# Optimization experiments

Hardware: AMD Instinct MI355X
Metric: run time of the kernel (lower is better)

Reference implementation:

```python
import jax, jax.numpy as jnp
import numpy as np

B, L, D = 1, 4096, 1024
N_AR, N_DIFF, D_HEAD = 8, 8, 64
H = N_AR + N_DIFF
ROPE_BASE = 10000.0


def rotate_half(x):
    x1, x2 = jnp.split(x, 2, axis=-1)
    return jnp.concatenate([-x2, x1], axis=-1)


def rope_cos_sin(seq_len, d_head):
    inv_freq = 1.0 / (ROPE_BASE ** (jnp.arange(0, d_head, 2, dtype=jnp.float32) / d_head))
    t = jnp.arange(seq_len, dtype=jnp.float32)
    freqs = t[:, None] * inv_freq[None, :]          # [L, d_head//2]
    emb = jnp.concatenate([freqs, freqs], axis=-1)  # [L, d_head]
    return jnp.cos(emb), jnp.sin(emb)


def setup_inputs() -> dict:
    key = jax.random.key(0)
    ks = jax.random.split(key, 5)
    return {
        "hidden_states": jax.random.normal(ks[0], (B, L, D), dtype=jnp.float32),
        "Wq": jax.random.normal(ks[1], (D, H * D_HEAD), dtype=jnp.float32) * 0.02,
        "Wk": jax.random.normal(ks[2], (D, H * D_HEAD), dtype=jnp.float32) * 0.02,
        "Wv": jax.random.normal(ks[3], (D, H * D_HEAD), dtype=jnp.float32) * 0.02,
        "Wo": jax.random.normal(ks[4], (H * D_HEAD, D), dtype=jnp.float32) * 0.02,
    }


def _attend(q, k, v, mask):
    # q,k,v: [B, h, L, d]; mask: [L, L] additive
    scale = D_HEAD ** -0.5
    scores = jnp.einsum("bhqd,bhkd->bhqk", q, k) * scale + mask
    attn = jax.nn.softmax(scores.astype(jnp.float32), axis=-1).astype(q.dtype)
    return jnp.einsum("bhqk,bhkd->bhqd", attn, v)


def reference(hidden_states, Wq, Wk, Wv, Wo):
    b, l, _ = hidden_states.shape

    def heads(x, W):
        return (x @ W).reshape(b, l, H, D_HEAD).transpose(0, 2, 1, 3)  # [B,H,L,d]

    q = heads(hidden_states, Wq)
    k = heads(hidden_states, Wk)
    v = heads(hidden_states, Wv)

    cos, sin = rope_cos_sin(l, D_HEAD)  # [L, d]
    q = q * cos + rotate_half(q) * sin
    k = k * cos + rotate_half(k) * sin

    neg_inf = jnp.finfo(jnp.float32).min
    causal = jnp.where(jnp.tril(jnp.ones((l, l), dtype=bool)), 0.0, -jnp.inf).astype(jnp.float32)

    out_ar = _attend(q[:, :N_AR], k[:, :N_AR], v[:, :N_AR], causal)
    out_diff = _attend(q[:, N_AR:], k[:, N_AR:], v[:, N_AR:], jnp.zeros((l, l), jnp.float32))

    out = jnp.concatenate([out_ar, out_diff], axis=1)          # [B,H,L,d]
    out = out.transpose(0, 2, 1, 3).reshape(b, l, H * D_HEAD)  # [B,L,H*d]
    return out @ Wo
```

## Files before the change

kernel.cpp:

```cpp
#include <hip/hip_runtime.h>

#define LSEQ 4096
#define DMODEL 1024
#define HTOT 16
#define NAR 8
#define DHEAD 64
#define QKVS 3072

typedef unsigned short u16;
typedef unsigned int u32;
typedef __attribute__((ext_vector_type(8))) short bf16x8;
typedef __attribute__((ext_vector_type(4))) short bf16x4;
typedef __attribute__((ext_vector_type(4))) float f32x4;
typedef __attribute__((ext_vector_type(4))) unsigned int u32x4;

typedef __attribute__((address_space(1))) void gvoid;
typedef __attribute__((address_space(3))) void lvoid;

__device__ __forceinline__ void cp16(const void* g, void* l) {
    __builtin_amdgcn_global_load_lds((gvoid*)(void*)g, (lvoid*)l, 16, 0, 0);
}

__device__ __forceinline__ float bfs(u16 v) { return __uint_as_float((u32)v << 16); }
__device__ __forceinline__ u16 f2bf(float f) {
    u32 x = __float_as_uint(f);
    return (u16)((x + 0x7fffu + ((x >> 16) & 1u)) >> 16);
}
__device__ __forceinline__ u32 packtr(float lo, float hi) {
    return __builtin_amdgcn_perm(__float_as_uint(hi), __float_as_uint(lo), 0x07060302u);
}

__global__ __launch_bounds__(256) void transp_cvt3(
    const float* __restrict__ Wq, const float* __restrict__ Wk,
    const float* __restrict__ Wv, u16* __restrict__ D)
{
    __shared__ u16 T[64][72];
    const float* S = (blockIdx.z == 0) ? Wq : ((blockIdx.z == 1) ? Wk : Wv);
    u16* Dz = D + (size_t)blockIdx.z * 1024 * 1024;
    const int tid = threadIdx.x;
    const int bx = blockIdx.x, by = blockIdx.y;
#pragma unroll
    for (int i = 0; i < 4; ++i) {
        int id = tid + i * 256;
        int fr = id >> 4, fc = id & 15;
        float4 v = *(const float4*)(S + (size_t)(by * 64 + fr) * 1024 + bx * 64 + fc * 4);
        T[fc * 4 + 0][fr] = f2bf(v.x);
        T[fc * 4 + 1][fr] = f2bf(v.y);
        T[fc * 4 + 2][fr] = f2bf(v.z);
        T[fc * 4 + 3][fr] = f2bf(v.w);
    }
    __syncthreads();
#pragma unroll
    for (int i = 0; i < 2; ++i) {
        int id = tid + i * 256;
        int c = id >> 3, g = id & 7;
        *(uint4*)(Dz + (size_t)(bx * 64 + c) * 1024 + by * 64 + g * 8) = *(const uint4*)&T[c][g * 8];
    }
}

__global__ __launch_bounds__(256) void transp_cvt(
    const float* __restrict__ S, u16* __restrict__ D)
{
    __shared__ u16 T[64][72];
    const int tid = threadIdx.x;
    const int bx = blockIdx.x, by = blockIdx.y;
#pragma unroll
    for (int i = 0; i < 4; ++i) {
        int id = tid + i * 256;
        int fr = id >> 4, fc = id & 15;
        float4 v = *(const float4*)(S + (size_t)(by * 64 + fr) * 1024 + bx * 64 + fc * 4);
        T[fc * 4 + 0][fr] = f2bf(v.x);
        T[fc * 4 + 1][fr] = f2bf(v.y);
        T[fc * 4 + 2][fr] = f2bf(v.z);
        T[fc * 4 + 3][fr] = f2bf(v.w);
    }
    __syncthreads();
#pragma unroll
    for (int i = 0; i < 2; ++i) {
        int id = tid + i * 256;
        int c = id >> 3, g = id & 7;
        *(uint4*)(D + (size_t)(bx * 64 + c) * 1024 + by * 64 + g * 8) = *(const uint4*)&T[c][g * 8];
    }
}

__global__ __launch_bounds__(256) void gemm_qkv(
    const float* __restrict__ A, const u16* __restrict__ Bt, u16* __restrict__ C)
{
    __shared__ u16 As[2][128][40];
    __shared__ u16 Bs[2][128][32];
    const int tid = threadIdx.x;
    const int lane = tid & 63, w = tid >> 6;
    const int col = lane & 15, quad = lane >> 4;
    const int bm = blockIdx.y << 7, bn = blockIdx.x << 7;
    const int wm = (w & 1) << 6, wn = (w >> 1) << 6;
    const int sr = lane >> 2, sc = (lane & 3) << 3;
    const int ar0 = tid >> 2, ag = (tid & 3) << 3;
    const f32x4 zero = {0.f, 0.f, 0.f, 0.f};
    f32x4 acc[4][4];
#pragma unroll
    for (int i = 0; i < 4; ++i)
#pragma unroll
        for (int j = 0; j < 4; ++j) acc[i][j] = zero;

    {
#pragma unroll
        for (int i = 0; i < 2; ++i)
            cp16(Bt + (size_t)(bn + w * 32 + i * 16 + sr) * 1024 + sc, &Bs[0][w * 32 + i * 16][0]);
#pragma unroll
        for (int it = 0; it < 2; ++it) {
            const float* ap = A + (size_t)(bm + ar0 + it * 64) * 1024 + ag;
            float4 a0 = *(const float4*)ap;
            float4 a1 = *(const float4*)(ap + 4);
            uint4 pk;
            pk.x = packtr(a0.x, a0.y); pk.y = packtr(a0.z, a0.w);
            pk.z = packtr(a1.x, a1.y); pk.w = packtr(a1.z, a1.w);
            *(uint4*)&As[0][ar0 + it * 64][ag] = pk;
        }
    }

    for (int kc = 0; kc < 32; ++kc) {
        const int cur = kc & 1, nxt = cur ^ 1;
        __syncthreads();
        const bool pre = (kc + 1 < 32);
        float4 a0[2], a1[2];
        if (pre) {
            const int k1 = (kc + 1) * 32;
#pragma unroll
            for (int i = 0; i < 2; ++i)
                cp16(Bt + (size_t)(bn + w * 32 + i * 16 + sr) * 1024 + k1 + sc,
                     &Bs[nxt][w * 32 + i * 16][0]);
#pragma unroll
            for (int it = 0; it < 2; ++it) {
                const float* ap = A + (size_t)(bm + ar0 + it * 64) * 1024 + k1 + ag;
                a0[it] = *(const float4*)ap;
                a1[it] = *(const float4*)(ap + 4);
            }
        }
        bf16x8 af[4], bfr[4];
#pragma unroll
        for (int i = 0; i < 4; ++i) af[i] = *(const bf16x8*)&As[cur][wm + i * 16 + col][quad * 8];
#pragma unroll
        for (int j = 0; j < 4; ++j) bfr[j] = *(const bf16x8*)&Bs[cur][wn + j * 16 + col][quad * 8];
#pragma unroll
        for (int i = 0; i < 4; ++i)
#pragma unroll
            for (int j = 0; j < 4; ++j)
                acc[i][j] = __builtin_amdgcn_mfma_f32_16x16x32_bf16(af[i], bfr[j], acc[i][j], 0, 0, 0);
        if (pre) {
#pragma unroll
            for (int it = 0; it < 2; ++it) {
                uint4 pk;
                pk.x = packtr(a0[it].x, a0[it].y); pk.y = packtr(a0[it].z, a0[it].w);
                pk.z = packtr(a1[it].x, a1[it].y); pk.w = packtr(a1[it].z, a1[it].w);
                *(uint4*)&As[nxt][ar0 + it * 64][ag] = pk;
            }
        }
    }

    if (blockIdx.x < 16) {
        const float scale = (blockIdx.x < 8) ? 0.18033688011112042f : 1.0f;
        const float inv0 = __expf((float)col * -0.2878231366242557f);
        const float inv1 = __expf((float)(16 + col) * -0.2878231366242557f);
#pragma unroll
        for (int i = 0; i < 4; ++i)
#pragma unroll
            for (int r = 0; r < 4; ++r) {
                const float t = (float)(bm + wm + i * 16 + quad * 4 + r);
                float s0, c0, s1, c1;
                __sincosf(t * inv0, &s0, &c0);
                __sincosf(t * inv1, &s1, &c1);
                float a0 = acc[i][0][r], b0 = acc[i][2][r];
                acc[i][0][r] = (a0 * c0 - b0 * s0) * scale;
                acc[i][2][r] = (b0 * c0 + a0 * s0) * scale;
                float a1 = acc[i][1][r], b1 = acc[i][3][r];
                acc[i][1][r] = (a1 * c1 - b1 * s1) * scale;
                acc[i][3][r] = (b1 * c1 + a1 * s1) * scale;
            }
    }
#pragma unroll
    for (int i = 0; i < 4; ++i)
#pragma unroll
        for (int j = 0; j < 4; ++j)
#pragma unroll
            for (int r = 0; r < 4; ++r)
                C[(size_t)(bm + wm + i * 16 + quad * 4 + r) * QKVS + bn + wn + j * 16 + col] =
                    f2bf(acc[i][j][r]);
}

__global__ __launch_bounds__(256) void gemm_out(
    const u16* __restrict__ A, const u16* __restrict__ Bt, float* __restrict__ C)
{
    __shared__ u16 As[2][128][32];
    __shared__ u16 Bs[2][128][32];
    const int tid = threadIdx.x;
    const int lane = tid & 63, w = tid >> 6;
    const int col = lane & 15, quad = lane >> 4;
    const int bm = blockIdx.y << 7, bn = blockIdx.x << 7;
    const int wm = (w & 1) << 6, wn = (w >> 1) << 6;
    const int sr = lane >> 2, sc = (lane & 3) << 3;
    const f32x4 zero = {0.f, 0.f, 0.f, 0.f};
    f32x4 acc[4][4];
#pragma unroll
    for (int i = 0; i < 4; ++i)
#pragma unroll
        for (int j = 0; j < 4; ++j) acc[i][j] = zero;

#pragma unroll
    for (int i = 0; i < 2; ++i) {
        const int r0 = w * 32 + i * 16;
        cp16(A  + (size_t)(bm + r0 + sr) * 1024 + sc, &As[0][r0][0]);
        cp16(Bt + (size_t)(bn + r0 + sr) * 1024 + sc, &Bs[0][r0][0]);
    }

    for (int kc = 0; kc < 32; ++kc) {
        const int cur = kc & 1, nxt = cur ^ 1;
        __syncthreads();
        if (kc + 1 < 32) {
            const int k1 = (kc + 1) * 32;
#pragma unroll
            for (int i = 0; i < 2; ++i) {
                const int r0 = w * 32 + i * 16;
                cp16(A  + (size_t)(bm + r0 + sr) * 1024 + k1 + sc, &As[nxt][r0][0]);
                cp16(Bt + (size_t)(bn + r0 + sr) * 1024 + k1 + sc, &Bs[nxt][r0][0]);
            }
        }
        bf16x8 af[4], bfr[4];
#pragma unroll
        for (int i = 0; i < 4; ++i) af[i] = *(const bf16x8*)&As[cur][wm + i * 16 + col][quad * 8];
#pragma unroll
        for (int j = 0; j < 4; ++j) bfr[j] = *(const bf16x8*)&Bs[cur][wn + j * 16 + col][quad * 8];
#pragma unroll
        for (int i = 0; i < 4; ++i)
#pragma unroll
            for (int j = 0; j < 4; ++j)
                acc[i][j] = __builtin_amdgcn_mfma_f32_16x16x32_bf16(af[i], bfr[j], acc[i][j], 0, 0, 0);
    }
#pragma unroll
    for (int i = 0; i < 4; ++i)
#pragma unroll
        for (int j = 0; j < 4; ++j)
#pragma unroll
            for (int r = 0; r < 4; ++r)
                C[(size_t)(bm + wm + i * 16 + quad * 4 + r) * 1024 + bn + wn + j * 16 + col] =
                    acc[i][j][r];
}

__global__ __launch_bounds__(256) void attn_mfma(
    const u16* __restrict__ QKV, u16* __restrict__ AO)
{
    __shared__ u16 Ks[2][128][64];
    __shared__ u16 Vt[2][64][136];
    const int bid = blockIdx.x;
    int h, qt;
    if (bid < 256) { h = 8 + (bid & 7); qt = bid >> 3; }
    else { int i = bid - 256; h = i & 7; qt = 31 - (i >> 3); }
    const bool causal = (h < NAR);
    const int tid = threadIdx.x;
    const int w = tid >> 6, lane = tid & 63;
    const int col = lane & 15, quad = lane >> 4;
    const int qb = qt * 128;
    const int qr0 = qb + w * 32 + col;
    const int qr1 = qr0 + 16;
    const int cva = ((lane >> 1) & 3) * 32 + (lane >> 3) * 4 + (lane & 1) * 2;

    bf16x8 qf[2][2];
#pragma unroll
    for (int s = 0; s < 2; ++s)
#pragma unroll
        for (int ks = 0; ks < 2; ++ks)
            qf[s][ks] = *(const bf16x8*)(QKV + (size_t)(qr0 + s * 16) * QKVS +
                                         h * DHEAD + ks * 32 + quad * 8);

    bf16x8 ones8;
#pragma unroll
    for (int i = 0; i < 8; ++i) ones8[i] = (short)0x3F80;

    const f32x4 zero = {0.f, 0.f, 0.f, 0.f};
    f32x4 O[2][5];
#pragma unroll
    for (int s = 0; s < 2; ++s)
#pragma unroll
        for (int nd = 0; nd < 5; ++nd) O[s][nd] = zero;

    const int nch = causal ? (qt + 1) : (LSEQ / 128);
    const int krow = lane >> 3;
    const int kcb = (lane & 7) ^ krow;
    const u16* kbase = QKV + (size_t)krow * QKVS + 1024 + h * DHEAD + kcb * 8;
    const u16* vbase = QKV + (size_t)(lane * 2) * QKVS + 2048 + h * DHEAD + w * 16;

    u32x4 vA0, vA1, vB0, vB1;
    bf16x8 pf8[2][4];

#define VT_WRITE(CUR)                                                                              \
    _Pragma("unroll")                                                                              \
    for (int j = 0; j < 4; ++j) {                                                                  \
        *(u32*)&Vt[CUR][w * 16 + 2 * j][cva]         = __builtin_amdgcn_perm(vB0[j], vA0[j], 0x05040100u); \
        *(u32*)&Vt[CUR][w * 16 + 2 * j + 1][cva]     = __builtin_amdgcn_perm(vB0[j], vA0[j], 0x07060302u); \
        *(u32*)&Vt[CUR][w * 16 + 8 + 2 * j][cva]     = __builtin_amdgcn_perm(vB1[j], vA1[j], 0x05040100u); \
        *(u32*)&Vt[CUR][w * 16 + 8 + 2 * j + 1][cva] = __builtin_amdgcn_perm(vB1[j], vA1[j], 0x07060302u); \
    }

#define PV_STEP(PRV)                                                                               \
    {                                                                                              \
        __builtin_amdgcn_s_setprio(1);                                                             \
        _Pragma("unroll")                                                                          \
        for (int tp = 0; tp < 4; ++tp) {                                                           \
            bf16x8 vv[4];                                                                          \
            _Pragma("unroll")                                                                      \
            for (int nd = 0; nd < 4; ++nd)                                                         \
                vv[nd] = *(const bf16x8*)&Vt[PRV][nd * 16 + col][quad * 32 + tp * 8];              \
            _Pragma("unroll")                                                                      \
            for (int nd = 0; nd < 4; ++nd) {                                                       \
                O[0][nd] = __builtin_amdgcn_mfma_f32_16x16x32_bf16(vv[nd], pf8[0][tp], O[0][nd], 0, 0, 0); \
                O[1][nd] = __builtin_amdgcn_mfma_f32_16x16x32_bf16(vv[nd], pf8[1][tp], O[1][nd], 0, 0, 0); \
            }                                                                                      \
            O[0][4] = __builtin_amdgcn_mfma_f32_16x16x32_bf16(ones8, pf8[0][tp], O[0][4], 0, 0, 0); \
            O[1][4] = __builtin_amdgcn_mfma_f32_16x16x32_bf16(ones8, pf8[1][tp], O[1][4], 0, 0, 0); \
        }                                                                                          \
        __builtin_amdgcn_s_setprio(0);                                                             \
    }

#define S_STEP(KBUF, CH)                                                                           \
    {                                                                                              \
        const bool mask = causal && ((CH) == qt);                                                  \
        _Pragma("unroll")                                                                          \
        for (int hf = 0; hf < 2; ++hf) {                                                           \
            f32x4 st[2][4];                                                                        \
            _Pragma("unroll")                                                                      \
            for (int s = 0; s < 2; ++s)                                                            \
                _Pragma("unroll")                                                                  \
                for (int jj = 0; jj < 4; ++jj) st[s][jj] = zero;                                   \
            __builtin_amdgcn_s_setprio(1);                                                         \
            _Pragma("unroll")                                                                      \
            for (int ks = 0; ks < 2; ++ks)                                                         \
                _Pragma("unroll")                                                                  \
                for (int jj = 0; jj < 4; ++jj) {                                                   \
                    bf16x8 kf = *(const bf16x8*)&Ks[KBUF][(hf * 4 + jj) * 16 + col]                \
                                                         [((ks * 4 + quad) ^ (col & 7)) * 8];      \
                    st[0][jj] = __builtin_amdgcn_mfma_f32_16x16x32_bf16(kf, qf[0][ks], st[0][jj], 0, 0, 0); \
                    st[1][jj] = __builtin_amdgcn_mfma_f32_16x16x32_bf16(kf, qf[1][ks], st[1][jj], 0, 0, 0); \
                }                                                                                  \
            __builtin_amdgcn_s_setprio(0);                                                         \
            if (mask) {                                                                            \
                _Pragma("unroll")                                                                  \
                for (int jj = 0; jj < 4; ++jj) {                                                   \
                    const int kk = (CH) * 128 + (hf * 4 + jj) * 16 + quad * 4;                     \
                    _Pragma("unroll")                                                              \
                    for (int r = 0; r < 4; ++r) {                                                  \
                        if (kk + r > qr0) st[0][jj][r] = -1e30f;                                   \
                        if (kk + r > qr1) st[1][jj][r] = -1e30f;                                   \
                    }                                                                              \
                }                                                                                  \
            }                                                                                      \
            _Pragma("unroll")                                                                      \
            for (int s = 0; s < 2; ++s)                                                            \
                _Pragma("unroll")                                                                  \
                for (int jj = 0; jj < 4; ++jj) {                                                   \
                    u32 plo = packtr(__builtin_amdgcn_exp2f(st[s][jj][0]),                         \
                                     __builtin_amdgcn_exp2f(st[s][jj][1]));                        \
                    u32 phi = packtr(__builtin_amdgcn_exp2f(st[s][jj][2]),                         \
                                     __builtin_amdgcn_exp2f(st[s][jj][3]));                        \
                    u32* p = (u32*)&pf8[s][0] + (hf * 4 + jj) * 2;                                 \
                    p[0] = plo; p[1] = phi;                                                        \
                }                                                                                  \
        }                                                                                          \
    }

#pragma unroll
    for (int i = 0; i < 4; ++i)
        cp16(kbase + (size_t)((i * 4 + w) * 8) * QKVS, &Ks[0][(i * 4 + w) * 8][0]);
    vA0 = *(u32x4*)(vbase);
    vA1 = *(u32x4*)(vbase + 8);
    vB0 = *(u32x4*)(vbase + QKVS);
    vB1 = *(u32x4*)(vbase + QKVS + 8);
    __syncthreads();
    VT_WRITE(0);
    if (nch > 1) {
#pragma unroll
        for (int i = 0; i < 4; ++i)
            cp16(kbase + (size_t)(128 + (i * 4 + w) * 8) * QKVS, &Ks[1][(i * 4 + w) * 8][0]);
        const u16* vp = vbase + (size_t)128 * QKVS;
        vA0 = *(u32x4*)(vp);
        vA1 = *(u32x4*)(vp + 8);
        vB0 = *(u32x4*)(vp + QKVS);
        vB1 = *(u32x4*)(vp + QKVS + 8);
    }
    S_STEP(0, 0);

    for (int ch = 1; ch < nch; ++ch) {
        const int cur = ch & 1, prv = cur ^ 1;
        __syncthreads();
        VT_WRITE(cur);
        if (ch + 1 < nch) {
            const size_t c1 = (size_t)(ch + 1) * 128;
#pragma unroll
            for (int i = 0; i < 4; ++i)
                cp16(kbase + (c1 + (i * 4 + w) * 8) * QKVS, &Ks[prv][(i * 4 + w) * 8][0]);
            const u16* vp = vbase + c1 * QKVS;
            vA0 = *(u32x4*)(vp);
            vA1 = *(u32x4*)(vp + 8);
            vB0 = *(u32x4*)(vp + QKVS);
            vB1 = *(u32x4*)(vp + QKVS + 8);
        }
        PV_STEP(prv);
        S_STEP(cur, ch);
    }

    __syncthreads();
    {
        const int prv = (nch - 1) & 1;
        PV_STEP(prv);
    }
#pragma unroll
    for (int s = 0; s < 2; ++s) {
        const float inv = 1.f / O[s][4][0];
        const int qrow = qr0 + s * 16;
#pragma unroll
        for (int nd = 0; nd < 4; ++nd) {
            ushort4 ov;
            ov.x = f2bf(O[s][nd][0] * inv);
            ov.y = f2bf(O[s][nd][1] * inv);
            ov.z = f2bf(O[s][nd][2] * inv);
            ov.w = f2bf(O[s][nd][3] * inv);
            *(ushort4*)(AO + (size_t)qrow * 1024 + h * DHEAD + nd * 16 + quad * 4) = ov;
        }
    }
#undef VT_WRITE
#undef PV_STEP
#undef S_STEP
}

extern "C" void kernel_launch(void* const* d_in, const int* in_sizes, int n_in,
                              void* d_out, int out_size, void* d_ws, size_t ws_size,
                              hipStream_t stream)
{
    const float* X  = (const float*)d_in[0];
    const float* Wq = (const float*)d_in[1];
    const float* Wk = (const float*)d_in[2];
    const float* Wv = (const float*)d_in[3];
    const float* Wo = (const float*)d_in[4];
    float* out = (float*)d_out;

    u16* Wt  = (u16*)d_ws;
    u16* AOb = (u16*)d_ws;
    u16* QKV = (u16*)d_ws + (size_t)4 * 1024 * 1024;
    u16* Wot = QKV;

    transp_cvt3<<<dim3(16, 16, 3), 256, 0, stream>>>(Wq, Wk, Wv, Wt);
    gemm_qkv<<<dim3(24, 32), 256, 0, stream>>>(X, Wt, QKV);
    attn_mfma<<<512, 256, 0, stream>>>(QKV, AOb);
    transp_cvt<<<dim3(16, 16), 256, 0, stream>>>(Wo, Wot);
    gemm_out<<<dim3(8, 32), 256, 0, stream>>>(AOb, Wot, out);
}
```

Measured before the change: 246.5 us.

## Split attention over key chunks and combine partials with atomics

The attention grid is split along the key dimension into groups of 8 chunks, so each block handles a slice of keys for one head and query tile. Unnormalized partial outputs and row sums are accumulated with float atomicAdd into scratch buffers (the output buffer is reused as scratch), and a new finalize kernel normalizes and converts them to bf16. The goal is more blocks and better load balance for the causal heads. In exchange it adds zeroing, copy and finalize launches plus heavy atomic traffic. It also accumulates without a running max, so it relies on the existing kernel's softmax scheme being safe across split partials.

```diff
diff --git a/kernel.cpp b/kernel.cpp
--- a/kernel.cpp
+++ b/kernel.cpp
@@ -245,15 +245,55 @@
                     acc[i][j][r];
 }
 
+__global__ __launch_bounds__(256) void zero_scratch(float* __restrict__ op, float* __restrict__ lb)
+{
+    const int i = blockIdx.x * 256 + threadIdx.x;
+    const float4 z = {0.f, 0.f, 0.f, 0.f};
+    if (i < 1024 * 1024) *(float4*)(op + (size_t)i * 4) = z;
+    if (i < 16 * 4096 / 4) *(float4*)(lb + (size_t)i * 4) = z;
+}
+
+__global__ __launch_bounds__(256) void copy_l(const float* __restrict__ src, float* __restrict__ dst)
+{
+    const int i = blockIdx.x * 256 + threadIdx.x;
+    if (i < 16 * 4096) dst[i] = src[i];
+}
+
+__global__ __launch_bounds__(256) void finalize_attn(
+    const float* __restrict__ OP, const float* __restrict__ lb, u16* __restrict__ AO)
+{
+    const int id = blockIdx.x * 256 + threadIdx.x;
+    const int q = id >> 7, g = id & 127;
+    const int dh0 = g * 8;
+    const float invl = 1.f / lb[(dh0 >> 6) * 4096 + q];
+    u32 pk[4];
+#pragma unroll
+    for (int k = 0; k < 4; ++k) {
+        float lo = OP[(size_t)(dh0 + 2 * k) * 4096 + q] * invl;
+        float hi = OP[(size_t)(dh0 + 2 * k + 1) * 4096 + q] * invl;
+        pk[k] = ((u32)f2bf(lo)) | (((u32)f2bf(hi)) << 16);
+    }
+    uint4 o; o.x = pk[0]; o.y = pk[1]; o.z = pk[2]; o.w = pk[3];
+    *(uint4*)(AO + (size_t)q * 1024 + dh0) = o;
+}
+
 __global__ __launch_bounds__(256) void attn_mfma(
-    const u16* __restrict__ QKV, u16* __restrict__ AO)
+    const u16* __restrict__ QKV, float* __restrict__ OP, float* __restrict__ lb)
 {
     __shared__ u16 Ks[2][128][64];
     __shared__ u16 Vt[2][64][136];
     const int bid = blockIdx.x;
-    int h, qt;
-    if (bid < 256) { h = 8 + (bid & 7); qt = bid >> 3; }
-    else { int i = bid - 256; h = i & 7; qt = 31 - (i >> 3); }
+    int h, qt, c0, c1;
+    if (bid < 1024) {
+        h = 8 + (bid & 7); qt = (bid >> 3) & 31;
+        c0 = (bid >> 8) * 8; c1 = c0 + 8;
+    } else {
+        const int i = bid - 1024;
+        h = i & 7; qt = 31 - ((i >> 3) & 31);
+        c0 = (i >> 8) * 8;
+        if (c0 > qt) return;
+        c1 = (c0 + 8 < qt + 1) ? (c0 + 8) : (qt + 1);
+    }
     const bool causal = (h < NAR);
     const int tid = threadIdx.x;
     const int w = tid >> 6, lane = tid & 63;
@@ -282,7 +322,6 @@
 #pragma unroll
         for (int nd = 0; nd < 5; ++nd) O[s][nd] = zero;
 
-    const int nch = causal ? (qt + 1) : (LSEQ / 128);
     const int krow = lane >> 3;
     const int kcb = (lane & 7) ^ krow;
     const u16* kbase = QKV + (size_t)krow * QKVS + 1024 + h * DHEAD + kcb * 8;
@@ -368,35 +407,38 @@
 
 #pragma unroll
     for (int i = 0; i < 4; ++i)
-        cp16(kbase + (size_t)((i * 4 + w) * 8) * QKVS, &Ks[0][(i * 4 + w) * 8][0]);
-    vA0 = *(u32x4*)(vbase);
-    vA1 = *(u32x4*)(vbase + 8);
-    vB0 = *(u32x4*)(vbase + QKVS);
-    vB1 = *(u32x4*)(vbase + QKVS + 8);
-    __syncthreads();
-    VT_WRITE(0);
-    if (nch > 1) {
-#pragma unroll
-        for (int i = 0; i < 4; ++i)
-            cp16(kbase + (size_t)(128 + (i * 4 + w) * 8) * QKVS, &Ks[1][(i * 4 + w) * 8][0]);
-        const u16* vp = vbase + (size_t)128 * QKVS;
+        cp16(kbase + (size_t)(c0 * 128 + (i * 4 + w) * 8) * QKVS, &Ks[0][(i * 4 + w) * 8][0]);
+    {
+        const u16* vp = vbase + (size_t)c0 * 128 * QKVS;
         vA0 = *(u32x4*)(vp);
         vA1 = *(u32x4*)(vp + 8);
         vB0 = *(u32x4*)(vp + QKVS);
         vB1 = *(u32x4*)(vp + QKVS + 8);
     }
-    S_STEP(0, 0);
-
-    for (int ch = 1; ch < nch; ++ch) {
+    __syncthreads();
+    VT_WRITE(0);
+    if (c1 - c0 > 1) {
+#pragma unroll
+        for (int i = 0; i < 4; ++i)
+            cp16(kbase + (size_t)((c0 + 1) * 128 + (i * 4 + w) * 8) * QKVS, &Ks[1][(i * 4 + w) * 8][0]);
+        const u16* vp = vbase + (size_t)(c0 + 1) * 128 * QKVS;
+        vA0 = *(u32x4*)(vp);
+        vA1 = *(u32x4*)(vp + 8);
+        vB0 = *(u32x4*)(vp + QKVS);
+        vB1 = *(u32x4*)(vp + QKVS + 8);
+    }
+    S_STEP(0, c0);
+
+    for (int ch = c0 + 1; ch < c1; ++ch) {
         const int cur = ch & 1, prv = cur ^ 1;
         __syncthreads();
         VT_WRITE(cur);
-        if (ch + 1 < nch) {
-            const size_t c1 = (size_t)(ch + 1) * 128;
+        if (ch + 1 < c1) {
+            const size_t cc = (size_t)(ch + 1) * 128;
 #pragma unroll
             for (int i = 0; i < 4; ++i)
-                cp16(kbase + (c1 + (i * 4 + w) * 8) * QKVS, &Ks[prv][(i * 4 + w) * 8][0]);
-            const u16* vp = vbase + c1 * QKVS;
+                cp16(kbase + (cc + (i * 4 + w) * 8) * QKVS, &Ks[prv][(i * 4 + w) * 8][0]);
+            const u16* vp = vbase + cc * QKVS;
             vA0 = *(u32x4*)(vp);
             vA1 = *(u32x4*)(vp + 8);
             vB0 = *(u32x4*)(vp + QKVS);
@@ -408,22 +450,18 @@
 
     __syncthreads();
     {
-        const int prv = (nch - 1) & 1;
+        const int prv = (c1 - 1) & 1;
         PV_STEP(prv);
     }
 #pragma unroll
     for (int s = 0; s < 2; ++s) {
-        const float inv = 1.f / O[s][4][0];
-        const int qrow = qr0 + s * 16;
-#pragma unroll
-        for (int nd = 0; nd < 4; ++nd) {
-            ushort4 ov;
-            ov.x = f2bf(O[s][nd][0] * inv);
-            ov.y = f2bf(O[s][nd][1] * inv);
-            ov.z = f2bf(O[s][nd][2] * inv);
-            ov.w = f2bf(O[s][nd][3] * inv);
-            *(ushort4*)(AO + (size_t)qrow * 1024 + h * DHEAD + nd * 16 + quad * 4) = ov;
-        }
+        const int q = qr0 + s * 16;
+#pragma unroll
+        for (int nd = 0; nd < 4; ++nd)
+#pragma unroll
+            for (int r = 0; r < 4; ++r)
+                atomicAdd(&OP[(size_t)(h * 64 + nd * 16 + quad * 4 + r) * 4096 + q], O[s][nd][r]);
+        if (quad == 0) atomicAdd(&lb[h * 4096 + q], O[s][4][0]);
     }
 #undef VT_WRITE
 #undef PV_STEP
@@ -443,12 +481,18 @@
 
     u16* Wt  = (u16*)d_ws;
     u16* AOb = (u16*)d_ws;
+    float* lA = (float*)((u16*)d_ws + (size_t)3 * 1024 * 1024);
     u16* QKV = (u16*)d_ws + (size_t)4 * 1024 * 1024;
     u16* Wot = QKV;
-
+    float* lB = (float*)((u16*)d_ws + (size_t)5 * 1024 * 1024);
+    float* OP = out;
+
+    zero_scratch<<<4096, 256, 0, stream>>>(OP, lA);
     transp_cvt3<<<dim3(16, 16, 3), 256, 0, stream>>>(Wq, Wk, Wv, Wt);
     gemm_qkv<<<dim3(24, 32), 256, 0, stream>>>(X, Wt, QKV);
-    attn_mfma<<<512, 256, 0, stream>>>(QKV, AOb);
+    attn_mfma<<<2048, 256, 0, stream>>>(QKV, OP, lA);
+    copy_l<<<256, 256, 0, stream>>>(lA, lB);
     transp_cvt<<<dim3(16, 16), 256, 0, stream>>>(Wo, Wot);
+    finalize_attn<<<2048, 256, 0, stream>>>(OP, lB, AOb);
     gemm_out<<<dim3(8, 32), 256, 0, stream>>>(AOb, Wot, out);
 }
```

Result: slower. 306.7 us (+24.4%).

## Single-buffer the transposed V tile in attention to cut LDS usage

Applied to the files above, without the earlier changes.

Collapses the double-buffered Vt shared-memory array into one buffer. The V loads for the current chunk are now issued inside the loop, and the transpose-write happens after S_STEP behind an extra barrier. Shared memory per block drops from about 67KB to about 50KB, which may let more blocks fit per CU. In exchange each iteration gains a second __syncthreads, and the V global-load latency is less hidden because it now overlaps only PV and S instead of a whole iteration.

```diff
diff --git a/kernel.cpp b/kernel.cpp
--- a/kernel.cpp
+++ b/kernel.cpp
@@ -21,7 +21,6 @@
     __builtin_amdgcn_global_load_lds((gvoid*)(void*)g, (lvoid*)l, 16, 0, 0);
 }
 
-__device__ __forceinline__ float bfs(u16 v) { return __uint_as_float((u32)v << 16); }
 __device__ __forceinline__ u16 f2bf(float f) {
     u32 x = __float_as_uint(f);
     return (u16)((x + 0x7fffu + ((x >> 16) & 1u)) >> 16);
@@ -249,7 +248,7 @@
     const u16* __restrict__ QKV, u16* __restrict__ AO)
 {
     __shared__ u16 Ks[2][128][64];
-    __shared__ u16 Vt[2][64][136];
+    __shared__ u16 Vt[64][136];
     const int bid = blockIdx.x;
     int h, qt;
     if (bid < 256) { h = 8 + (bid & 7); qt = bid >> 3; }
@@ -291,16 +290,16 @@
     u32x4 vA0, vA1, vB0, vB1;
     bf16x8 pf8[2][4];
 
-#define VT_WRITE(CUR)                                                                              \
+#define VT_WRITE()                                                                                 \
     _Pragma("unroll")                                                                              \
     for (int j = 0; j < 4; ++j) {                                                                  \
-        *(u32*)&Vt[CUR][w * 16 + 2 * j][cva]         = __builtin_amdgcn_perm(vB0[j], vA0[j], 0x05040100u); \
-        *(u32*)&Vt[CUR][w * 16 + 2 * j + 1][cva]     = __builtin_amdgcn_perm(vB0[j], vA0[j], 0x07060302u); \
-        *(u32*)&Vt[CUR][w * 16 + 8 + 2 * j][cva]     = __builtin_amdgcn_perm(vB1[j], vA1[j], 0x05040100u); \
-        *(u32*)&Vt[CUR][w * 16 + 8 + 2 * j + 1][cva] = __builtin_amdgcn_perm(vB1[j], vA1[j], 0x07060302u); \
-    }
-
-#define PV_STEP(PRV)                                                                               \
+        *(u32*)&Vt[w * 16 + 2 * j][cva]         = __builtin_amdgcn_perm(vB0[j], vA0[j], 0x05040100u); \
+        *(u32*)&Vt[w * 16 + 2 * j + 1][cva]     = __builtin_amdgcn_perm(vB0[j], vA0[j], 0x07060302u); \
+        *(u32*)&Vt[w * 16 + 8 + 2 * j][cva]     = __builtin_amdgcn_perm(vB1[j], vA1[j], 0x05040100u); \
+        *(u32*)&Vt[w * 16 + 8 + 2 * j + 1][cva] = __builtin_amdgcn_perm(vB1[j], vA1[j], 0x07060302u); \
+    }
+
+#define PV_STEP()                                                                                  \
     {                                                                                              \
         __builtin_amdgcn_s_setprio(1);                                                             \
         _Pragma("unroll")                                                                          \
@@ -308,7 +307,7 @@
             bf16x8 vv[4];                                                                          \
             _Pragma("unroll")                                                                      \
             for (int nd = 0; nd < 4; ++nd)                                                         \
-                vv[nd] = *(const bf16x8*)&Vt[PRV][nd * 16 + col][quad * 32 + tp * 8];              \
+                vv[nd] = *(const bf16x8*)&Vt[nd * 16 + col][quad * 32 + tp * 8];                   \
             _Pragma("unroll")                                                                      \
             for (int nd = 0; nd < 4; ++nd) {                                                       \
                 O[0][nd] = __builtin_amdgcn_mfma_f32_16x16x32_bf16(vv[nd], pf8[0][tp], O[0][nd], 0, 0, 0); \
@@ -374,43 +373,39 @@
     vB0 = *(u32x4*)(vbase + QKVS);
     vB1 = *(u32x4*)(vbase + QKVS + 8);
     __syncthreads();
-    VT_WRITE(0);
+    VT_WRITE();
     if (nch > 1) {
 #pragma unroll
         for (int i = 0; i < 4; ++i)
             cp16(kbase + (size_t)(128 + (i * 4 + w) * 8) * QKVS, &Ks[1][(i * 4 + w) * 8][0]);
-        const u16* vp = vbase + (size_t)128 * QKVS;
-        vA0 = *(u32x4*)(vp);
-        vA1 = *(u32x4*)(vp + 8);
-        vB0 = *(u32x4*)(vp + QKVS);
-        vB1 = *(u32x4*)(vp + QKVS + 8);
     }
     S_STEP(0, 0);
 
     for (int ch = 1; ch < nch; ++ch) {
-        const int cur = ch & 1, prv = cur ^ 1;
+        const int cur = ch & 1;
         __syncthreads();
-        VT_WRITE(cur);
         if (ch + 1 < nch) {
             const size_t c1 = (size_t)(ch + 1) * 128;
 #pragma unroll
             for (int i = 0; i < 4; ++i)
-                cp16(kbase + (c1 + (i * 4 + w) * 8) * QKVS, &Ks[prv][(i * 4 + w) * 8][0]);
-            const u16* vp = vbase + c1 * QKVS;
+                cp16(kbase + (c1 + (i * 4 + w) * 8) * QKVS, &Ks[cur ^ 1][(i * 4 + w) * 8][0]);
+        }
+        {
+            const u16* vp = vbase + (size_t)ch * 128 * QKVS;
             vA0 = *(u32x4*)(vp);
             vA1 = *(u32x4*)(vp + 8);
             vB0 = *(u32x4*)(vp + QKVS);
             vB1 = *(u32x4*)(vp + QKVS + 8);
         }
-        PV_STEP(prv);
+        PV_STEP();
         S_STEP(cur, ch);
+        __syncthreads();
+        VT_WRITE();
     }
 
     __syncthreads();
-    {
-        const int prv = (nch - 1) & 1;
-        PV_STEP(prv);
-    }
+    PV_STEP();
+
 #pragma unroll
     for (int s = 0; s < 2; ++s) {
         const float inv = 1.f / O[s][4][0];
```

After: 245.1 us. About the same (-0.6%).
